# Kernel optimization log

Measured on AMD Instinct MI355X. Metric: run time of the kernel, lower is better.

The kernel has to match this reference:

```python
import jax, jax.numpy as jnp
import numpy as np

THRESHOLD = 1.0  # max tolerable Sampson error (px^2), as in the docstring example scale


def _normalize(pts, w):
    # pts: (B, M, 3) homogeneous points, w: (B, M) 0/1 weights.
    # Hartley normalization: centroid -> origin, mean distance -> sqrt(2).
    ws = w.sum(-1, keepdims=True)                                   # (B, 1)
    mean = (pts[..., :2] * w[..., None]).sum(-2) / ws               # (B, 2)
    d = jnp.linalg.norm(pts[..., :2] - mean[..., None, :], axis=-1)  # (B, M)
    md = (d * w).sum(-1) / ws[..., 0]                               # (B,)
    s = jnp.sqrt(2.0) / (md + 1e-8)
    z, o = jnp.zeros_like(s), jnp.ones_like(s)
    T = jnp.stack([
        jnp.stack([s, z, -s * mean[..., 0]], -1),
        jnp.stack([z, s, -s * mean[..., 1]], -1),
        jnp.stack([z, z, o], -1)], -2)                              # (B, 3, 3)
    return pts @ jnp.swapaxes(T, -1, -2), T


def eight_point(p1, p2, w):
    # Weighted normalized 8-point algorithm. p1, p2: (B, M, 3); w: (B, M).
    # Zero-weight rows contribute nothing to A^T A, so this equals fitting on the
    # selected subset (as the original does by fancy-indexing inlier rows).
    p1n, T1 = _normalize(p1, w)
    p2n, T2 = _normalize(p2, w)
    A = (p2n[..., :, None] * p1n[..., None, :]).reshape(p1.shape[:-2] + (-1, 9))
    A = A * w[..., None]                                            # (B, M, 9)
    AtA = jnp.einsum('...mi,...mj->...ij', A, A)                    # (B, 9, 9)
    _, V = jnp.linalg.eigh(AtA)                                     # ascending eigvals
    F = V[..., :, 0].reshape(p1.shape[:-2] + (3, 3))                # null vector
    U, S, Vt = jnp.linalg.svd(F, full_matrices=False)               # enforce rank 2
    F = (U * S.at[..., -1].set(0.0)[..., None, :]) @ Vt
    F = jnp.swapaxes(T2, -1, -2) @ F @ T1                           # denormalize
    return F / F[..., 2:3, 2:3]


def sampson_error(p1, p2, F):
    # p1, p2: (N, 3); F: (B, 3, 3) -> err: (B, N)
    Fx1 = jnp.einsum('bij,nj->bni', F, p1)
    Ftx2 = jnp.einsum('bij,ni->bnj', F, p2)
    num = jnp.einsum('ni,bni->bn', p2, Fx1) ** 2
    den = Fx1[..., 0] ** 2 + Fx1[..., 1] ** 2 + Ftx2[..., 0] ** 2 + Ftx2[..., 1] ** 2
    return num / den


def setup_inputs() -> dict:
    N, ITERS, K = 16384, 4096, 8
    rng = np.random.default_rng(0)
    X = rng.uniform(-2.0, 2.0, (N, 3)); X[:, 2] += 6.0               # 3D points, depth ~[4, 8]
    Kmat = np.array([[500.0, 0.0, 256.0], [0.0, 500.0, 256.0], [0.0, 0.0, 1.0]])
    th = 0.1
    R = np.array([[np.cos(th), 0.0, np.sin(th)], [0.0, 1.0, 0.0], [-np.sin(th), 0.0, np.cos(th)]])
    t = np.array([0.5, 0.1, 0.0])
    x1 = X @ Kmat.T; x1 /= x1[:, 2:]
    X2 = X @ R.T + t
    x2 = X2 @ Kmat.T; x2 /= x2[:, 2:]
    x1[:, :2] += rng.normal(0.0, 0.3, (N, 2))
    x2[:, :2] += rng.normal(0.0, 0.3, (N, 2))
    out = rng.random(N) < 0.3
    x2[out, :2] = rng.uniform(0.0, 512.0, (int(out.sum()), 2))
    samples = jax.random.randint(jax.random.key(0), (ITERS, K), 0, N, dtype=jnp.int32)
    return {"pts1": jnp.asarray(x1, jnp.float32), "pts2": jnp.asarray(x2, jnp.float32),
            "samples": samples, "iterations": ITERS, "num_of_select": K}


def reference(pts1, pts2, samples, iterations, num_of_select):
    samples = samples[:iterations, :num_of_select]                   # (B, 8), static slice
    # uniqueness check per hypothesis row (original drops non-unique rows; we mask them)
    srt = jnp.sort(samples, axis=-1)
    uniq = jnp.all(srt[:, 1:] != srt[:, :-1], axis=-1)               # (B,)
    p1s, p2s = pts1[samples], pts2[samples]                          # (B, 8, 3)
    w1 = jnp.ones(samples.shape, pts1.dtype)
    F = eight_point(p1s, p2s, w1)                                    # (B, 3, 3)
    err = sampson_error(pts1, pts2, F)                               # (B, N)
    inl = err <= THRESHOLD
    ml = inl.sum(-1).astype(pts1.dtype)                              # mask_lens
    ml_max = jnp.max(jnp.where(uniq, ml, 0.0))
    mask_len_ratio = ml / ml_max
    # sqrt of inlier errors; safe-guard masked entries so sqrt grad stays finite
    sqrt_sum = (jnp.sqrt(jnp.where(inl, err, 1.0)) * inl).sum(-1)
    means = (sqrt_sum + 1e-8) / (ml + 1e-8)
    means_max = jnp.max(jnp.where(uniq, means, -jnp.inf))
    score = 0.5 * mask_len_ratio + 0.5 * (1.0 - means / means_max)
    best = jnp.argmax(jnp.where(uniq, score, -jnp.inf))
    wbest = inl[best].astype(pts1.dtype)                             # (N,)
    Mbest = eight_point(pts1[None], pts2[None], wbest[None])[0]      # refit on inliers
    return Mbest, inl[best]
```

## Files before the change

kernel.cpp:

```cpp
#include <hip/hip_runtime.h>
#include <math.h>
#include <type_traits>
#include <utility>

#if defined(__has_builtin)
#if __has_builtin(__builtin_amdgcn_rcpf)
#define FAST_RCPF(x) __builtin_amdgcn_rcpf(x)
#endif
#if __has_builtin(__builtin_amdgcn_rsqf)
#define FAST_RSQF(x) __builtin_amdgcn_rsqf(x)
#endif
#endif
#ifndef FAST_RCPF
#define FAST_RCPF(x) (1.0f / (x))
#endif
#ifndef FAST_RSQF
#define FAST_RSQF(x) (1.0f / sqrtf(x))
#endif

__host__ __device__ constexpr int PIX(int i, int j) { return i * (i + 1) / 2 + j; }

template <int N, int I = 0, typename F>
__device__ __forceinline__ void static_for(F&& f) {
  if constexpr (I < N) {
    f(std::integral_constant<int, I>{});
    static_for<N, I + 1>(static_cast<F&&>(f));
  }
}

template <int I, int J, int K>
__device__ __forceinline__ double csub9(const double* M, double s) {
  if constexpr (K >= J) return s;
  else return csub9<I, J, K + 1>(M, s - M[PIX(I, K)] * M[PIX(J, K)]);
}
template <int I, int J>
__device__ __forceinline__ void cholJ(double* M) {
  if constexpr (J <= I) {
    double s = csub9<I, J, 0>(M, M[PIX(I, J)]);
    if constexpr (J == I)
      M[PIX(I, I)] = sqrt(fmax(s, 1e-300));
    else
      M[PIX(I, J)] = s / M[PIX(J, J)];
    cholJ<I, J + 1>(M);
  }
}
template <int I>
__device__ __forceinline__ void cholI(double* M) {
  if constexpr (I < 9) {
    cholJ<I, 0>(M);
    cholI<I + 1>(M);
  }
}

template <int I, int K>
__device__ __forceinline__ double fsub9(const double* L, const double* x, double s) {
  if constexpr (K >= I) return s;
  else return fsub9<I, K + 1>(L, x, s - L[PIX(I, K)] * x[K]);
}
template <int I>
__device__ __forceinline__ void fwd9(const double* L, double* x) {
  if constexpr (I < 9) {
    x[I] = fsub9<I, 0>(L, x, x[I]) / L[PIX(I, I)];
    fwd9<I + 1>(L, x);
  }
}
template <int I, int K>
__device__ __forceinline__ double bsub9(const double* L, const double* x, double s) {
  if constexpr (K >= 9) return s;
  else return bsub9<I, K + 1>(L, x, s - L[PIX(K, I)] * x[K]);
}
template <int I>
__device__ __forceinline__ void bwd9(const double* L, double* x) {
  if constexpr (I >= 0) {
    x[I] = bsub9<I, I + 1>(L, x, x[I]) / L[PIX(I, I)];
    bwd9<I - 1>(L, x);
  }
}

template <int I, int J>
__device__ __forceinline__ void ataIJ(double* M, const double (&a)[9], double w) {
  if constexpr (J <= I) {
    M[PIX(I, J)] += w * a[I] * a[J];
    ataIJ<I, J + 1>(M, a, w);
  }
}
template <int I>
__device__ __forceinline__ void ataI(double* M, const double (&a)[9], double w) {
  if constexpr (I < 9) {
    ataIJ<I, 0>(M, a, w);
    ataI<I + 1>(M, a, w);
  }
}

#define JROT(P, Q)                                                              \
  {                                                                             \
    double apq = a##P##Q;                                                       \
    if (fabs(apq) >= 1e-300) {                                                  \
      double tau = (a##Q##Q - a##P##P) / (2.0 * apq);                           \
      double t = ((tau >= 0.0) ? 1.0 : -1.0) / (fabs(tau) + sqrt(1.0 + tau * tau)); \
      double c = 1.0 / sqrt(1.0 + t * t);                                       \
      double s = t * c;                                                         \
      double t0p = a0##P, t0q = a0##Q;                                          \
      a0##P = c * t0p - s * t0q; a0##Q = s * t0p + c * t0q;                     \
      double t1p = a1##P, t1q = a1##Q;                                          \
      a1##P = c * t1p - s * t1q; a1##Q = s * t1p + c * t1q;                     \
      double t2p = a2##P, t2q = a2##Q;                                          \
      a2##P = c * t2p - s * t2q; a2##Q = s * t2p + c * t2q;                     \
      double rp0 = a##P##0, rq0 = a##Q##0;                                      \
      a##P##0 = c * rp0 - s * rq0; a##Q##0 = s * rp0 + c * rq0;                 \
      double rp1 = a##P##1, rq1 = a##Q##1;                                      \
      a##P##1 = c * rp1 - s * rq1; a##Q##1 = s * rp1 + c * rq1;                 \
      double rp2 = a##P##2, rq2 = a##Q##2;                                      \
      a##P##2 = c * rp2 - s * rq2; a##Q##2 = s * rp2 + c * rq2;                 \
      double u0p = V0##P, u0q = V0##Q;                                          \
      V0##P = c * u0p - s * u0q; V0##Q = s * u0p + c * u0q;                     \
      double u1p = V1##P, u1q = V1##Q;                                          \
      V1##P = c * u1p - s * u1q; V1##Q = s * u1p + c * u1q;                     \
      double u2p = V2##P, u2q = V2##Q;                                          \
      V2##P = c * u2p - s * u2q; V2##Q = s * u2p + c * u2q;                     \
    }                                                                           \
  }

__device__ __forceinline__ void solveF(double* M, double s1, double m1x, double m1y,
                                       double s2, double m2x, double m2y,
                                       float* out) {
  double tr = M[0] + M[2] + M[5] + M[9] + M[14] + M[20] + M[27] + M[35] + M[44];
  double shift = 1e-12 * tr;
  M[0] += shift; M[2] += shift; M[5] += shift; M[9] += shift; M[14] += shift;
  M[20] += shift; M[27] += shift; M[35] += shift; M[44] += shift;
  cholI<0>(M);
  double x[9];
  static_for<9>([&](auto i) { x[i] = 1.0; });
  static_for<3>([&](auto) {
    fwd9<0>(M, x);
    bwd9<8>(M, x);
    double n = 0.0;
    static_for<9>([&](auto i) { n += x[i] * x[i]; });
    n = 1.0 / sqrt(n);
    static_for<9>([&](auto i) { x[i] *= n; });
  });
  const double g00 = x[0] * x[0] + x[3] * x[3] + x[6] * x[6];
  const double g01 = x[0] * x[1] + x[3] * x[4] + x[6] * x[7];
  const double g02 = x[0] * x[2] + x[3] * x[5] + x[6] * x[8];
  const double g11 = x[1] * x[1] + x[4] * x[4] + x[7] * x[7];
  const double g12 = x[1] * x[2] + x[4] * x[5] + x[7] * x[8];
  const double g22 = x[2] * x[2] + x[5] * x[5] + x[8] * x[8];
  double a00 = g00, a01 = g01, a02 = g02;
  double a10 = g01, a11 = g11, a12 = g12;
  double a20 = g02, a21 = g12, a22 = g22;
  double V00 = 1, V01 = 0, V02 = 0;
  double V10 = 0, V11 = 1, V12 = 0;
  double V20 = 0, V21 = 0, V22 = 1;
  for (int sweep = 0; sweep < 6; ++sweep) {
    JROT(0, 1);
    JROT(0, 2);
    JROT(1, 2);
  }
  double mv = a00, v0 = V00, v1 = V10, v2 = V20;
  if (a11 < mv) { mv = a11; v0 = V01; v1 = V11; v2 = V21; }
  if (a22 < mv) { mv = a22; v0 = V02; v1 = V12; v2 = V22; }
  const double fv0 = x[0] * v0 + x[1] * v1 + x[2] * v2;
  const double fv1 = x[3] * v0 + x[4] * v1 + x[5] * v2;
  const double fv2 = x[6] * v0 + x[7] * v1 + x[8] * v2;
  const double F200 = x[0] - fv0 * v0, F201 = x[1] - fv0 * v1, F202 = x[2] - fv0 * v2;
  const double F210 = x[3] - fv1 * v0, F211 = x[4] - fv1 * v1, F212 = x[5] - fv1 * v2;
  const double F220 = x[6] - fv2 * v0, F221 = x[7] - fv2 * v1, F222 = x[8] - fv2 * v2;
  const double R00 = s2 * F200, R01 = s2 * F201, R02 = s2 * F202;
  const double R10 = s2 * F210, R11 = s2 * F211, R12 = s2 * F212;
  const double R20 = -s2 * m2x * F200 - s2 * m2y * F210 + F220;
  const double R21 = -s2 * m2x * F201 - s2 * m2y * F211 + F221;
  const double R22 = -s2 * m2x * F202 - s2 * m2y * F212 + F222;
  const double Ff00 = s1 * R00, Ff01 = s1 * R01;
  const double Ff02 = -s1 * m1x * R00 - s1 * m1y * R01 + R02;
  const double Ff10 = s1 * R10, Ff11 = s1 * R11;
  const double Ff12 = -s1 * m1x * R10 - s1 * m1y * R11 + R12;
  const double Ff20 = s1 * R20, Ff21 = s1 * R21;
  const double Ff22 = -s1 * m1x * R20 - s1 * m1y * R21 + R22;
  const double inv = 1.0 / Ff22;
  out[0] = (float)(Ff00 * inv); out[1] = (float)(Ff01 * inv); out[2] = (float)(Ff02 * inv);
  out[3] = (float)(Ff10 * inv); out[4] = (float)(Ff11 * inv); out[5] = (float)(Ff12 * inv);
  out[6] = (float)(Ff20 * inv); out[7] = (float)(Ff21 * inv); out[8] = (float)(Ff22 * inv);
}

struct F9 {
  float f0, f1, f2, f3, f4, f5, f6, f7, f8;
};

__device__ __forceinline__ F9 loadF(const float* __restrict__ p) {
  F9 F;
  F.f0 = p[0]; F.f1 = p[1]; F.f2 = p[2];
  F.f3 = p[3]; F.f4 = p[4]; F.f5 = p[5];
  F.f6 = p[6]; F.f7 = p[7]; F.f8 = p[8];
  return F;
}

__device__ __forceinline__ void samp_numden(const F9& F, float px, float py,
                                            float qx, float qy, float& num,
                                            float& den, float& dout) {
  float a0 = fmaf(F.f0, px, fmaf(F.f1, py, F.f2));
  float a1 = fmaf(F.f3, px, fmaf(F.f4, py, F.f5));
  float a2 = fmaf(F.f6, px, fmaf(F.f7, py, F.f8));
  float b0 = fmaf(F.f0, qx, fmaf(F.f3, qy, F.f6));
  float b1 = fmaf(F.f1, qx, fmaf(F.f4, qy, F.f7));
  float d = fmaf(qx, a0, fmaf(qy, a1, a2));
  num = d * d;
  den = fmaf(a0, a0, fmaf(a1, a1, fmaf(b0, b0, b1 * b1)));
  dout = d;
}

__device__ __forceinline__ void samp_acc(const F9& F, float px, float py,
                                         float qx, float qy, float& cnt,
                                         float& ss) {
  float num, den, d;
  samp_numden(F, px, py, qx, qy, num, den, d);
  const bool in = (num <= den);
  const float val = fabsf(d) * FAST_RSQF(den);
  cnt += in ? 1.0f : 0.0f;
  ss += in ? val : 0.0f;
}

__global__ __launch_bounds__(256, 1) void prep_and_fit(
    const float* __restrict__ pts1, const float* __restrict__ pts2,
    const int* __restrict__ samples, float4* __restrict__ P1,
    float4* __restrict__ P2, float* __restrict__ models,
    int* __restrict__ uflag, double* __restrict__ acc, int N, int iters,
    int TB) {
  if ((int)blockIdx.x < TB) {
    if (blockIdx.x == 0 && threadIdx.x < 52) acc[threadIdx.x] = 0.0;
    const int i = blockIdx.x * 256 + threadIdx.x;
    if (i < N) {
      P1[i] = make_float4(pts1[3 * i], pts1[3 * i + 1], pts1[3 * i + 2], 0.f);
      P2[i] = make_float4(pts2[3 * i], pts2[3 * i + 1], pts2[3 * i + 2], 0.f);
    }
    return;
  }
  if (threadIdx.x >= 64) return;
  const int it = (blockIdx.x - TB) * 64 + threadIdx.x;
  if (it >= iters) return;

  int idx[8];
  static_for<8>([&](auto k) { idx[k] = samples[it * 8 + k]; });
  int u = 1;
  static_for<8>([&](auto A) {
    static_for<8>([&](auto B) {
      if constexpr (decltype(B)::value > decltype(A)::value) {
        if (idx[A] == idx[B]) u = 0;
      }
    });
  });
  uflag[it] = u;

  float X1[8], Y1[8], Z1[8], X2[8], Y2[8], Z2[8];
  static_for<8>([&](auto k) {
    const int j = idx[k];
    X1[k] = pts1[3 * j]; Y1[k] = pts1[3 * j + 1]; Z1[k] = pts1[3 * j + 2];
    X2[k] = pts2[3 * j]; Y2[k] = pts2[3 * j + 1]; Z2[k] = pts2[3 * j + 2];
  });
  double sx1 = 0, sy1 = 0, sx2 = 0, sy2 = 0;
  static_for<8>([&](auto k) {
    sx1 += (double)X1[k]; sy1 += (double)Y1[k];
    sx2 += (double)X2[k]; sy2 += (double)Y2[k];
  });
  const double m1x = sx1 / 8.0, m1y = sy1 / 8.0;
  const double m2x = sx2 / 8.0, m2y = sy2 / 8.0;
  double sd1 = 0, sd2 = 0;
  static_for<8>([&](auto k) {
    double dx1 = (double)X1[k] - m1x, dy1 = (double)Y1[k] - m1y;
    double dx2 = (double)X2[k] - m2x, dy2 = (double)Y2[k] - m2y;
    sd1 += sqrt(dx1 * dx1 + dy1 * dy1);
    sd2 += sqrt(dx2 * dx2 + dy2 * dy2);
  });
  const double s1 = sqrt(2.0) / (sd1 / 8.0 + 1e-8);
  const double s2 = sqrt(2.0) / (sd2 / 8.0 + 1e-8);

  double M[45];
  static_for<45>([&](auto r) { M[r] = 0.0; });
  static_for<8>([&](auto k) {
    const double z1 = (double)Z1[k], z2 = (double)Z2[k];
    const double p1x = s1 * ((double)X1[k] - m1x * z1);
    const double p1y = s1 * ((double)Y1[k] - m1y * z1);
    const double p2x = s2 * ((double)X2[k] - m2x * z2);
    const double p2y = s2 * ((double)Y2[k] - m2y * z2);
    const double a[9] = {p2x * p1x, p2x * p1y, p2x * z1,
                         p2y * p1x, p2y * p1y, p2y * z1,
                         z2 * p1x,  z2 * p1y,  z2 * z1};
    ataI<0>(M, a, 1.0);
  });
  solveF(M, s1, m1x, m1y, s2, m2x, m2y, models + (size_t)it * 9);
}

__global__ __launch_bounds__(256, 4) void sampson_stats4(
    const float4* __restrict__ P1, const float4* __restrict__ P2,
    const float* __restrict__ models, float* __restrict__ ml,
    float* __restrict__ ssum, int N, int iters) {
  const int m0 = blockIdx.x * 4;
  const int c0 = min(m0 + 0, iters - 1), c1 = min(m0 + 1, iters - 1);
  const int c2 = min(m0 + 2, iters - 1), c3 = min(m0 + 3, iters - 1);
  const F9 Fa = loadF(models + (size_t)c0 * 9);
  const F9 Fb = loadF(models + (size_t)c1 * 9);
  const F9 Fc = loadF(models + (size_t)c2 * 9);
  const F9 Fd = loadF(models + (size_t)c3 * 9);
  float ca = 0, cb = 0, cc = 0, cd = 0;
  float sa = 0, sb = 0, sc_ = 0, sd = 0;
  const int NP = N & ~511;
  for (int i = threadIdx.x; i < NP; i += 512) {
    const float4 pA = P1[i];
    const float4 qA = P2[i];
    const float4 pB = P1[i + 256];
    const float4 qB = P2[i + 256];
    samp_acc(Fa, pA.x, pA.y, qA.x, qA.y, ca, sa);
    samp_acc(Fb, pA.x, pA.y, qA.x, qA.y, cb, sb);
    samp_acc(Fc, pA.x, pA.y, qA.x, qA.y, cc, sc_);
    samp_acc(Fd, pA.x, pA.y, qA.x, qA.y, cd, sd);
    samp_acc(Fa, pB.x, pB.y, qB.x, qB.y, ca, sa);
    samp_acc(Fb, pB.x, pB.y, qB.x, qB.y, cb, sb);
    samp_acc(Fc, pB.x, pB.y, qB.x, qB.y, cc, sc_);
    samp_acc(Fd, pB.x, pB.y, qB.x, qB.y, cd, sd);
  }
  for (int i = NP + threadIdx.x; i < N; i += 256) {
    const float4 p = P1[i];
    const float4 q = P2[i];
    samp_acc(Fa, p.x, p.y, q.x, q.y, ca, sa);
    samp_acc(Fb, p.x, p.y, q.x, q.y, cb, sb);
    samp_acc(Fc, p.x, p.y, q.x, q.y, cc, sc_);
    samp_acc(Fd, p.x, p.y, q.x, q.y, cd, sd);
  }
  __shared__ float shc[4][4], shs[4][4];
  const int lane = threadIdx.x & 63, wv = threadIdx.x >> 6;
  float c4[4] = {ca, cb, cc, cd};
  float s4[4] = {sa, sb, sc_, sd};
  static_for<4>([&](auto m) {
    float c = c4[m], s = s4[m];
#pragma unroll
    for (int o = 32; o > 0; o >>= 1) {
      c += __shfl_down(c, o);
      s += __shfl_down(s, o);
    }
    if (lane == 0) { shc[wv][m] = c; shs[wv][m] = s; }
  });
  __syncthreads();
  if (threadIdx.x < 4 && m0 + threadIdx.x < iters) {
    const int m = threadIdx.x;
    ml[m0 + m] = shc[0][m] + shc[1][m] + shc[2][m] + shc[3][m];
    ssum[m0 + m] = shs[0][m] + shs[1][m] + shs[2][m] + shs[3][m];
  }
}

__global__ __launch_bounds__(256) void selmask_p1(
    const float4* __restrict__ P1, const float4* __restrict__ P2,
    const float* __restrict__ models, const float* __restrict__ ml,
    const float* __restrict__ ssum, const int* __restrict__ uniq,
    float* __restrict__ outmask, double* __restrict__ acc, int N, int iters) {
  const int tid = threadIdx.x;
  __shared__ float ra[256], rb[256];
  __shared__ int rid[256];
  float mlmax = 0.f, mnmax = -INFINITY;
  for (int i = tid; i < iters; i += 256) {
    if (uniq[i]) {
      float m = ml[i];
      mlmax = fmaxf(mlmax, m);
      float mean = (ssum[i] + 1e-8f) / (m + 1e-8f);
      mnmax = fmaxf(mnmax, mean);
    }
  }
  ra[tid] = mlmax;
  rb[tid] = mnmax;
  __syncthreads();
  for (int s = 128; s > 0; s >>= 1) {
    if (tid < s) {
      ra[tid] = fmaxf(ra[tid], ra[tid + s]);
      rb[tid] = fmaxf(rb[tid], rb[tid + s]);
    }
    __syncthreads();
  }
  const float MLMAX = ra[0];
  const float MNMAX = rb[0];
  __syncthreads();
  float bsc = -INFINITY;
  int bid = 0x7FFFFFFF;
  for (int i = tid; i < iters; i += 256) {
    float sc = -INFINITY;
    float m = ml[i];
    float mean = (ssum[i] + 1e-8f) / (m + 1e-8f);
    if (uniq[i]) sc = 0.5f * (m / MLMAX) + 0.5f * (1.0f - mean / MNMAX);
    if (sc > bsc || (sc == bsc && i < bid)) { bsc = sc; bid = i; }
  }
  ra[tid] = bsc;
  rid[tid] = bid;
  __syncthreads();
  for (int s = 128; s > 0; s >>= 1) {
    if (tid < s) {
      if (ra[tid + s] > ra[tid] ||
          (ra[tid + s] == ra[tid] && rid[tid + s] < rid[tid])) {
        ra[tid] = ra[tid + s];
        rid[tid] = rid[tid + s];
      }
    }
    __syncthreads();
  }
  const int best = rid[0];

  const int i = blockIdx.x * 256 + tid;
  double w = 0, a = 0, b = 0, c = 0, d = 0;
  if (i < N) {
    const F9 F = loadF(models + (size_t)best * 9);
    const float4 p = P1[i];
    const float4 q = P2[i];
    float num, den, dd;
    samp_numden(F, p.x, p.y, q.x, q.y, num, den, dd);
    const bool in = (num <= den);
    float m = in ? 1.0f : 0.0f;
    outmask[i] = m;
    w = (double)m;
    a = w * (double)p.x;
    b = w * (double)p.y;
    c = w * (double)q.x;
    d = w * (double)q.y;
  }
#pragma unroll
  for (int o = 32; o > 0; o >>= 1) {
    w += __shfl_down(w, o); a += __shfl_down(a, o); b += __shfl_down(b, o);
    c += __shfl_down(c, o); d += __shfl_down(d, o);
  }
  if ((tid & 63) == 0) {
    atomicAdd(&acc[0], w); atomicAdd(&acc[1], a); atomicAdd(&acc[2], b);
    atomicAdd(&acc[3], c); atomicAdd(&acc[4], d);
  }
}

__global__ __launch_bounds__(256, 1) void ff_p23(
    const float* __restrict__ mask, const float4* __restrict__ P1,
    const float4* __restrict__ P2, double* __restrict__ acc, int N) {
  const double WS = acc[0];
  const double M1X = acc[1] / WS, M1Y = acc[2] / WS;
  const double M2X = acc[3] / WS, M2Y = acc[4] / WS;
  double sd1 = 0, sd2 = 0;
  double A[45];
  static_for<45>([&](auto r) { A[r] = 0.0; });
#pragma unroll
  for (int k = 0; k < 4; ++k) {
    const int i = blockIdx.x * 1024 + k * 256 + threadIdx.x;
    if (i < N) {
      const double w = (double)mask[i];
      if (w != 0.0) {
        const float4 p = P1[i];
        const float4 q = P2[i];
        const double v0 = (double)p.x - M1X, v1 = (double)p.y - M1Y;
        const double u0 = (double)q.x - M2X, u1 = (double)q.y - M2Y;
        sd1 += sqrt(v0 * v0 + v1 * v1);
        sd2 += sqrt(u0 * u0 + u1 * u1);
        const double a[9] = {u0 * v0, u0 * v1, u0,
                             u1 * v0, u1 * v1, u1,
                             v0,      v1,      1.0};
        ataI<0>(A, a, 1.0);
      }
    }
  }
  const int lane = threadIdx.x & 63;
  {
    double t1 = sd1, t2 = sd2;
#pragma unroll
    for (int o = 32; o > 0; o >>= 1) {
      t1 += __shfl_down(t1, o);
      t2 += __shfl_down(t2, o);
    }
    if (lane == 0) {
      atomicAdd(&acc[5], t1);
      atomicAdd(&acc[6], t2);
    }
  }
  static_for<45>([&](auto r) {
    double v = A[r];
#pragma unroll
    for (int o = 32; o > 0; o >>= 1) v += __shfl_down(v, o);
    if (lane == 0) atomicAdd(&acc[7 + r], v);
  });
}

__global__ __launch_bounds__(64, 1) void ff_solve(const double* __restrict__ acc,
                                                  float* __restrict__ outF) {
  if (threadIdx.x != 0 || blockIdx.x != 0) return;
  const double WS = acc[0];
  const double M1X = acc[1] / WS, M1Y = acc[2] / WS;
  const double M2X = acc[3] / WS, M2Y = acc[4] / WS;
  const double S1 = sqrt(2.0) / (acc[5] / WS + 1e-8);
  const double S2 = sqrt(2.0) / (acc[6] / WS + 1e-8);
  double M[45];
  static_for<45>([&](auto r) { M[r] = acc[7 + r]; });
  static_for<9>([&](auto R) {
    static_for<9>([&](auto C) {
      constexpr int r = decltype(R)::value;
      constexpr int c = decltype(C)::value;
      if constexpr (c <= r) {
        const double sr = ((r / 3) < 2 ? S2 : 1.0) * ((r % 3) < 2 ? S1 : 1.0);
        const double sc = ((c / 3) < 2 ? S2 : 1.0) * ((c % 3) < 2 ? S1 : 1.0);
        M[PIX(r, c)] *= sr * sc;
      }
    });
  });
  solveF(M, S1, M1X, M1Y, S2, M2X, M2Y, outF);
}

extern "C" void kernel_launch(void* const* d_in, const int* in_sizes, int n_in,
                              void* d_out, int out_size, void* d_ws, size_t ws_size,
                              hipStream_t stream) {
  const float* pts1 = (const float*)d_in[0];
  const float* pts2 = (const float*)d_in[1];
  const int* samples = (const int*)d_in[2];
  const int N = in_sizes[0] / 3;
  const int iters = in_sizes[2] / 8;

  float4* P1 = (float4*)d_ws;
  float4* P2 = P1 + N;
  double* acc = (double*)(P2 + N);
  float* models = (float*)(acc + 52);
  float* ml = models + (size_t)iters * 9;
  float* ssum = ml + iters;
  int* uniq = (int*)(ssum + iters);

  float* outF = (float*)d_out;
  float* outmask = outF + 9;

  const int TB = (N + 255) / 256;
  const int FB = (iters + 63) / 64;
  prep_and_fit<<<TB + FB, 256, 0, stream>>>(pts1, pts2, samples, P1, P2,
                                            models, uniq, acc, N, iters, TB);
  sampson_stats4<<<(iters + 3) / 4, 256, 0, stream>>>(P1, P2, models, ml, ssum,
                                                      N, iters);
  selmask_p1<<<(N + 255) / 256, 256, 0, stream>>>(P1, P2, models, ml, ssum,
                                                  uniq, outmask, acc, N, iters);
  ff_p23<<<(N + 1023) / 1024, 256, 0, stream>>>(outmask, P1, P2, acc, N);
  ff_solve<<<1, 64, 0, stream>>>(acc, outF);
}
```

Measured before the change: 184.8 us.

## Drop float4 repack, fuse mask and moment accumulation via grid-wide spin barrier

Removes the point-repacking stage, so the fit kernel runs only 64-thread blocks and the Sampson scoring kernel reads the strided xyz inputs directly. The mask-selection and second-moment accumulation kernels are merged into one kernel that uses an atomic counter and a spin-wait flag to publish the inlier means before each block accumulates A^T A from registers. This saves a kernel launch plus the mask and point reloads. In exchange, the hot scoring loop uses uncoalesced stride-3 loads, and the spin barrier needs every block of the fused kernel to be co-resident to avoid deadlock.

```diff
diff --git a/kernel.cpp b/kernel.cpp
--- a/kernel.cpp
+++ b/kernel.cpp
@@ -219,23 +219,16 @@
   ss += in ? val : 0.0f;
 }
 
-__global__ __launch_bounds__(256, 1) void prep_and_fit(
+__global__ __launch_bounds__(64, 1) void fit_models(
     const float* __restrict__ pts1, const float* __restrict__ pts2,
-    const int* __restrict__ samples, float4* __restrict__ P1,
-    float4* __restrict__ P2, float* __restrict__ models,
-    int* __restrict__ uflag, double* __restrict__ acc, int N, int iters,
-    int TB) {
-  if ((int)blockIdx.x < TB) {
-    if (blockIdx.x == 0 && threadIdx.x < 52) acc[threadIdx.x] = 0.0;
-    const int i = blockIdx.x * 256 + threadIdx.x;
-    if (i < N) {
-      P1[i] = make_float4(pts1[3 * i], pts1[3 * i + 1], pts1[3 * i + 2], 0.f);
-      P2[i] = make_float4(pts2[3 * i], pts2[3 * i + 1], pts2[3 * i + 2], 0.f);
-    }
-    return;
-  }
-  if (threadIdx.x >= 64) return;
-  const int it = (blockIdx.x - TB) * 64 + threadIdx.x;
+    const int* __restrict__ samples, float* __restrict__ models,
+    int* __restrict__ uflag, double* __restrict__ acc,
+    unsigned int* __restrict__ sync2, int iters) {
+  if (blockIdx.x == 0) {
+    acc[threadIdx.x] = 0.0;
+    if (threadIdx.x == 0) { sync2[0] = 0u; sync2[1] = 0u; }
+  }
+  const int it = blockIdx.x * 64 + threadIdx.x;
   if (it >= iters) return;
 
   int idx[8];
@@ -290,7 +283,7 @@
 }
 
 __global__ __launch_bounds__(256, 4) void sampson_stats4(
-    const float4* __restrict__ P1, const float4* __restrict__ P2,
+    const float* __restrict__ pts1, const float* __restrict__ pts2,
     const float* __restrict__ models, float* __restrict__ ml,
     float* __restrict__ ssum, int N, int iters) {
   const int m0 = blockIdx.x * 4;
@@ -304,26 +297,27 @@
   float sa = 0, sb = 0, sc_ = 0, sd = 0;
   const int NP = N & ~511;
   for (int i = threadIdx.x; i < NP; i += 512) {
-    const float4 pA = P1[i];
-    const float4 qA = P2[i];
-    const float4 pB = P1[i + 256];
-    const float4 qB = P2[i + 256];
-    samp_acc(Fa, pA.x, pA.y, qA.x, qA.y, ca, sa);
-    samp_acc(Fb, pA.x, pA.y, qA.x, qA.y, cb, sb);
-    samp_acc(Fc, pA.x, pA.y, qA.x, qA.y, cc, sc_);
-    samp_acc(Fd, pA.x, pA.y, qA.x, qA.y, cd, sd);
-    samp_acc(Fa, pB.x, pB.y, qB.x, qB.y, ca, sa);
-    samp_acc(Fb, pB.x, pB.y, qB.x, qB.y, cb, sb);
-    samp_acc(Fc, pB.x, pB.y, qB.x, qB.y, cc, sc_);
-    samp_acc(Fd, pB.x, pB.y, qB.x, qB.y, cd, sd);
+    const int j = i + 256;
+    const float pxA = pts1[3 * i], pyA = pts1[3 * i + 1];
+    const float qxA = pts2[3 * i], qyA = pts2[3 * i + 1];
+    const float pxB = pts1[3 * j], pyB = pts1[3 * j + 1];
+    const float qxB = pts2[3 * j], qyB = pts2[3 * j + 1];
+    samp_acc(Fa, pxA, pyA, qxA, qyA, ca, sa);
+    samp_acc(Fb, pxA, pyA, qxA, qyA, cb, sb);
+    samp_acc(Fc, pxA, pyA, qxA, qyA, cc, sc_);
+    samp_acc(Fd, pxA, pyA, qxA, qyA, cd, sd);
+    samp_acc(Fa, pxB, pyB, qxB, qyB, ca, sa);
+    samp_acc(Fb, pxB, pyB, qxB, qyB, cb, sb);
+    samp_acc(Fc, pxB, pyB, qxB, qyB, cc, sc_);
+    samp_acc(Fd, pxB, pyB, qxB, qyB, cd, sd);
   }
   for (int i = NP + threadIdx.x; i < N; i += 256) {
-    const float4 p = P1[i];
-    const float4 q = P2[i];
-    samp_acc(Fa, p.x, p.y, q.x, q.y, ca, sa);
-    samp_acc(Fb, p.x, p.y, q.x, q.y, cb, sb);
-    samp_acc(Fc, p.x, p.y, q.x, q.y, cc, sc_);
-    samp_acc(Fd, p.x, p.y, q.x, q.y, cd, sd);
+    const float px = pts1[3 * i], py = pts1[3 * i + 1];
+    const float qx = pts2[3 * i], qy = pts2[3 * i + 1];
+    samp_acc(Fa, px, py, qx, qy, ca, sa);
+    samp_acc(Fb, px, py, qx, qy, cb, sb);
+    samp_acc(Fc, px, py, qx, qy, cc, sc_);
+    samp_acc(Fd, px, py, qx, qy, cd, sd);
   }
   __shared__ float shc[4][4], shs[4][4];
   const int lane = threadIdx.x & 63, wv = threadIdx.x >> 6;
@@ -346,11 +340,12 @@
   }
 }
 
-__global__ __launch_bounds__(256) void selmask_p1(
-    const float4* __restrict__ P1, const float4* __restrict__ P2,
+__global__ __launch_bounds__(256, 1) void selmask_final(
+    const float* __restrict__ pts1, const float* __restrict__ pts2,
     const float* __restrict__ models, const float* __restrict__ ml,
     const float* __restrict__ ssum, const int* __restrict__ uniq,
-    float* __restrict__ outmask, double* __restrict__ acc, int N, int iters) {
+    float* __restrict__ outmask, double* __restrict__ acc,
+    unsigned int* __restrict__ sync2, int N, int iters, int NB) {
   const int tid = threadIdx.x;
   __shared__ float ra[256], rb[256];
   __shared__ int rid[256];
@@ -401,62 +396,76 @@
   const int best = rid[0];
 
   const int i = blockIdx.x * 256 + tid;
-  double w = 0, a = 0, b = 0, c = 0, d = 0;
+  float px = 0.f, py = 0.f, qx = 0.f, qy = 0.f;
+  bool in = false;
   if (i < N) {
     const F9 F = loadF(models + (size_t)best * 9);
-    const float4 p = P1[i];
-    const float4 q = P2[i];
+    px = pts1[3 * i]; py = pts1[3 * i + 1];
+    qx = pts2[3 * i]; qy = pts2[3 * i + 1];
     float num, den, dd;
-    samp_numden(F, p.x, p.y, q.x, q.y, num, den, dd);
-    const bool in = (num <= den);
-    float m = in ? 1.0f : 0.0f;
-    outmask[i] = m;
-    w = (double)m;
-    a = w * (double)p.x;
-    b = w * (double)p.y;
-    c = w * (double)q.x;
-    d = w * (double)q.y;
-  }
+    samp_numden(F, px, py, qx, qy, num, den, dd);
+    in = (num <= den);
+    outmask[i] = in ? 1.0f : 0.0f;
+  }
+  {
+    double w = in ? 1.0 : 0.0;
+    double a = in ? (double)px : 0.0, b = in ? (double)py : 0.0;
+    double c = in ? (double)qx : 0.0, d = in ? (double)qy : 0.0;
 #pragma unroll
-  for (int o = 32; o > 0; o >>= 1) {
-    w += __shfl_down(w, o); a += __shfl_down(a, o); b += __shfl_down(b, o);
-    c += __shfl_down(c, o); d += __shfl_down(d, o);
-  }
-  if ((tid & 63) == 0) {
-    atomicAdd(&acc[0], w); atomicAdd(&acc[1], a); atomicAdd(&acc[2], b);
-    atomicAdd(&acc[3], c); atomicAdd(&acc[4], d);
-  }
-}
-
-__global__ __launch_bounds__(256, 1) void ff_p23(
-    const float* __restrict__ mask, const float4* __restrict__ P1,
-    const float4* __restrict__ P2, double* __restrict__ acc, int N) {
-  const double WS = acc[0];
-  const double M1X = acc[1] / WS, M1Y = acc[2] / WS;
-  const double M2X = acc[3] / WS, M2Y = acc[4] / WS;
+    for (int o = 32; o > 0; o >>= 1) {
+      w += __shfl_down(w, o); a += __shfl_down(a, o); b += __shfl_down(b, o);
+      c += __shfl_down(c, o); d += __shfl_down(d, o);
+    }
+    if ((tid & 63) == 0) {
+      atomicAdd(&acc[0], w); atomicAdd(&acc[1], a); atomicAdd(&acc[2], b);
+      atomicAdd(&acc[3], c); atomicAdd(&acc[4], d);
+    }
+  }
+  __syncthreads();
+  __shared__ int amLast;
+  if (tid == 0) {
+    __threadfence();
+    amLast = (atomicAdd(&sync2[0], 1u) == (unsigned int)(NB - 1)) ? 1 : 0;
+  }
+  __syncthreads();
+  if (amLast && tid == 0) {
+    const double WS = atomicAdd(&acc[0], 0.0);
+    acc[52] = atomicAdd(&acc[1], 0.0) / WS;
+    acc[53] = atomicAdd(&acc[2], 0.0) / WS;
+    acc[54] = atomicAdd(&acc[3], 0.0) / WS;
+    acc[55] = atomicAdd(&acc[4], 0.0) / WS;
+    __threadfence();
+    atomicExch(&sync2[1], 1u);
+  }
+  __shared__ double smean[4];
+  if (tid == 0) {
+    while (atomicAdd(&sync2[1], 0u) == 0u) {
+      __builtin_amdgcn_s_sleep(1);
+    }
+    __threadfence();
+    smean[0] = atomicAdd(&acc[52], 0.0);
+    smean[1] = atomicAdd(&acc[53], 0.0);
+    smean[2] = atomicAdd(&acc[54], 0.0);
+    smean[3] = atomicAdd(&acc[55], 0.0);
+  }
+  __syncthreads();
+  const double M1X = smean[0], M1Y = smean[1];
+  const double M2X = smean[2], M2Y = smean[3];
+
   double sd1 = 0, sd2 = 0;
   double A[45];
   static_for<45>([&](auto r) { A[r] = 0.0; });
-#pragma unroll
-  for (int k = 0; k < 4; ++k) {
-    const int i = blockIdx.x * 1024 + k * 256 + threadIdx.x;
-    if (i < N) {
-      const double w = (double)mask[i];
-      if (w != 0.0) {
-        const float4 p = P1[i];
-        const float4 q = P2[i];
-        const double v0 = (double)p.x - M1X, v1 = (double)p.y - M1Y;
-        const double u0 = (double)q.x - M2X, u1 = (double)q.y - M2Y;
-        sd1 += sqrt(v0 * v0 + v1 * v1);
-        sd2 += sqrt(u0 * u0 + u1 * u1);
-        const double a[9] = {u0 * v0, u0 * v1, u0,
-                             u1 * v0, u1 * v1, u1,
-                             v0,      v1,      1.0};
-        ataI<0>(A, a, 1.0);
-      }
-    }
-  }
-  const int lane = threadIdx.x & 63;
+  if (in) {
+    const double v0 = (double)px - M1X, v1 = (double)py - M1Y;
+    const double u0 = (double)qx - M2X, u1 = (double)qy - M2Y;
+    sd1 = sqrt(v0 * v0 + v1 * v1);
+    sd2 = sqrt(u0 * u0 + u1 * u1);
+    const double a[9] = {u0 * v0, u0 * v1, u0,
+                         u1 * v0, u1 * v1, u1,
+                         v0,      v1,      1.0};
+    ataI<0>(A, a, 1.0);
+  }
+  const int lane = tid & 63;
   {
     double t1 = sd1, t2 = sd2;
 #pragma unroll
@@ -510,10 +519,9 @@
   const int N = in_sizes[0] / 3;
   const int iters = in_sizes[2] / 8;
 
-  float4* P1 = (float4*)d_ws;
-  float4* P2 = P1 + N;
-  double* acc = (double*)(P2 + N);
-  float* models = (float*)(acc + 52);
+  double* acc = (double*)d_ws;
+  unsigned int* sync2 = (unsigned int*)(acc + 64);
+  float* models = (float*)(sync2 + 4);
   float* ml = models + (size_t)iters * 9;
   float* ssum = ml + iters;
   int* uniq = (int*)(ssum + iters);
@@ -521,14 +529,13 @@
   float* outF = (float*)d_out;
   float* outmask = outF + 9;
 
-  const int TB = (N + 255) / 256;
   const int FB = (iters + 63) / 64;
-  prep_and_fit<<<TB + FB, 256, 0, stream>>>(pts1, pts2, samples, P1, P2,
-                                            models, uniq, acc, N, iters, TB);
-  sampson_stats4<<<(iters + 3) / 4, 256, 0, stream>>>(P1, P2, models, ml, ssum,
-                                                      N, iters);
-  selmask_p1<<<(N + 255) / 256, 256, 0, stream>>>(P1, P2, models, ml, ssum,
-                                                  uniq, outmask, acc, N, iters);
-  ff_p23<<<(N + 1023) / 1024, 256, 0, stream>>>(outmask, P1, P2, acc, N);
+  const int NB = (N + 255) / 256;
+  fit_models<<<FB, 64, 0, stream>>>(pts1, pts2, samples, models, uniq, acc,
+                                    sync2, iters);
+  sampson_stats4<<<(iters + 3) / 4, 256, 0, stream>>>(pts1, pts2, models, ml,
+                                                      ssum, N, iters);
+  selmask_final<<<NB, 256, 0, stream>>>(pts1, pts2, models, ml, ssum, uniq,
+                                        outmask, acc, sync2, N, iters, NB);
   ff_solve<<<1, 64, 0, stream>>>(acc, outF);
 }
```

New measurement: 213.1 us. 15.3% more time.
